# Kernel optimization log

Hardware: AMD Instinct MI355X
Metric: run time of the kernel (lower is better)

The kernel has to match this reference:

```python
import jax, jax.numpy as jnp
import numpy as np

N = 102400      # total agents across all groups
GROUP = 50      # agents per group
G = N // GROUP  # 2048 groups
E = 128         # embedding_dim
H = 512         # h_dim


def setup_inputs() -> dict:
    key = jax.random.key(0)
    k1, k2, k3, k4, k5, k6 = jax.random.split(key, 6)
    hist_enc = jax.random.normal(k1, (N, H), dtype=jnp.float32)
    hist_pos_batch = jax.random.normal(k2, (N, 2), dtype=jnp.float32)
    # group boundaries: 0, 50, 100, ..., N  (len = G+1)
    seq_start_end = (jnp.arange(G + 1, dtype=jnp.int32) * GROUP)
    # spatial_embedding: Linear(2, E)
    Ws = jax.random.normal(k3, (2, E), dtype=jnp.float32) * (1.0 / np.sqrt(2.0))
    bs = jax.random.normal(k4, (E,), dtype=jnp.float32) * 0.01
    # mlp_pre_pool: Linear(E + H, H)
    Wm = jax.random.normal(k5, (E + H, H), dtype=jnp.float32) * (1.0 / np.sqrt(E + H))
    bm = jax.random.normal(k6, (H,), dtype=jnp.float32) * 0.01
    return {
        "hist_enc": hist_enc,
        "hist_pos_batch": hist_pos_batch,
        "seq_start_end": seq_start_end,
        "Ws": Ws, "bs": bs, "Wm": Wm, "bm": bm,
    }


def reference(hist_enc, hist_pos_batch, seq_start_end, Ws, bs, Wm, bm):
    # The original torch loop builds all n^2 pairs per group but keeps only
    # curr_pool_h[0:1], i.e. row i=0 -> pooled vector for the group's FIRST agent.
    # rel[i=0, j] = pos[j] - pos[start]; hidden index is j; max over j.
    n = hist_enc.shape[0]
    num_groups = seq_start_end.shape[0] - 1
    # segment id of each agent: group g covers [sse[g], sse[g+1])
    seg_ids = jnp.searchsorted(seq_start_end, jnp.arange(n, dtype=seq_start_end.dtype), side="right") - 1
    starts = seq_start_end[:-1]                      # [G]
    anchor = hist_pos_batch[starts][seg_ids]         # [N,2] pos of group's first agent
    rel = hist_pos_batch - anchor                    # [N,2]
    emb = jax.nn.relu(rel @ Ws + bs)                 # [N,E]
    h_in = jnp.concatenate([hist_enc, emb], axis=1)  # [N,E+H]
    pooled = jax.nn.relu(h_in @ Wm + bm)             # [N,H]
    out = jax.ops.segment_max(pooled, seg_ids, num_segments=num_groups)  # [G,H]
    return out
```

## Files before the change

kernel.cpp:

```cpp
#include <hip/hip_runtime.h>


typedef __bf16 bf16x8 __attribute__((ext_vector_type(8)));
typedef float floatx4 __attribute__((ext_vector_type(4)));

constexpr int NR = 102400;
constexpr int NG = 2048;
constexpr int E  = 128;
constexpr int H  = 512;
constexpr int KD = 640;
constexpr int BM = 128, BN = 128, BK = 32;

__device__ inline unsigned short f2bf(float f) {
    unsigned u = __float_as_uint(f);
    u += 0x7FFF + ((u >> 16) & 1u);
    return (unsigned short)(u >> 16);
}

__device__ inline void async16(const void* g, void* l) {
    __builtin_amdgcn_global_load_lds(
        (const __attribute__((address_space(1))) unsigned int*)g,
        (__attribute__((address_space(3))) unsigned int*)l, 16, 0, 0);
}

__global__ __launch_bounds__(256) void wm_transpose(const float* __restrict__ Wm,
                                                    unsigned short* __restrict__ WmT) {
    __shared__ float tile[64][65];
    const int kb = blockIdx.x * 64, nb = blockIdx.y * 64;
    const int tx = threadIdx.x & 63, tq = threadIdx.x >> 6;
#pragma unroll
    for (int i = 0; i < 16; ++i) {
        const int k = tq * 16 + i;
        tile[k][tx] = Wm[(size_t)(kb + k) * H + nb + tx];
    }
    __syncthreads();
#pragma unroll
    for (int i = 0; i < 16; ++i) {
        const int n = tq * 16 + i;
        WmT[(size_t)(nb + n) * KD + kb + tx] = f2bf(tile[tx][n]);
    }
}

__global__ __launch_bounds__(256) void build_a(
    const float* __restrict__ hist_enc, const float* __restrict__ pos,
    const int* __restrict__ sse, const float* __restrict__ Ws,
    const float* __restrict__ bs, unsigned short* __restrict__ Abf)
{
    __shared__ float relRow[BM][2];
    const int t = threadIdx.x;
    const int rowBase = blockIdx.x * BM;
    if (t < BM) {
        const int i = rowBase + t;
        int l = 0, r = NG + 1;
        while (l < r) { int m = (l + r) >> 1; if (sse[m] <= i) l = m + 1; else r = m; }
        const int a = sse[l - 1];
        relRow[t][0] = pos[2 * i + 0] - pos[2 * a + 0];
        relRow[t][1] = pos[2 * i + 1] - pos[2 * a + 1];
    }
    __syncthreads();
#pragma unroll 4
    for (int j = 0; j < 32; ++j) {
        const int c = j * 256 + t;
        const int row = c >> 6, col = (c & 63) * 8;
        const float4 f0 = *(const float4*)&hist_enc[(size_t)(rowBase + row) * H + col];
        const float4 f1 = *(const float4*)&hist_enc[(size_t)(rowBase + row) * H + col + 4];
        unsigned short ub[8] = {f2bf(f0.x), f2bf(f0.y), f2bf(f0.z), f2bf(f0.w),
                                f2bf(f1.x), f2bf(f1.y), f2bf(f1.z), f2bf(f1.w)};
        *(uint4*)&Abf[(size_t)(rowBase + row) * KD + col] = *(const uint4*)ub;
    }
#pragma unroll 2
    for (int j = 0; j < 8; ++j) {
        const int c = j * 256 + t;
        const int row = c >> 4, e = (c & 15) * 8;
        const float r0 = relRow[row][0], r1 = relRow[row][1];
        const float4 w0a = *(const float4*)&Ws[e],     w0b = *(const float4*)&Ws[e + 4];
        const float4 w1a = *(const float4*)&Ws[E + e], w1b = *(const float4*)&Ws[E + e + 4];
        const float4 ba  = *(const float4*)&bs[e],     bb  = *(const float4*)&bs[e + 4];
        unsigned short ub[8] = {
            f2bf(fmaxf(r0 * w0a.x + r1 * w1a.x + ba.x, 0.f)),
            f2bf(fmaxf(r0 * w0a.y + r1 * w1a.y + ba.y, 0.f)),
            f2bf(fmaxf(r0 * w0a.z + r1 * w1a.z + ba.z, 0.f)),
            f2bf(fmaxf(r0 * w0a.w + r1 * w1a.w + ba.w, 0.f)),
            f2bf(fmaxf(r0 * w0b.x + r1 * w1b.x + bb.x, 0.f)),
            f2bf(fmaxf(r0 * w0b.y + r1 * w1b.y + bb.y, 0.f)),
            f2bf(fmaxf(r0 * w0b.z + r1 * w1b.z + bb.z, 0.f)),
            f2bf(fmaxf(r0 * w0b.w + r1 * w1b.w + bb.w, 0.f))};
        *(uint4*)&Abf[(size_t)(rowBase + row) * KD + H + e] = *(const uint4*)ub;
    }
}

__global__ __launch_bounds__(256) void pool_mfma4(
    const unsigned short* __restrict__ Abf,
    const int*   __restrict__ sse,
    const unsigned short* __restrict__ WmT,
    const float* __restrict__ bm,
    float*       __restrict__ out)
{
    __shared__ __attribute__((aligned(16))) unsigned short As2[2][BM * BK];
    __shared__ __attribute__((aligned(16))) unsigned short Bs2[2][BN * BK];
    __shared__ int segRow[BM];
    __shared__ int bnd[3];
    __shared__ int Pmax[4][BN + 4];

    const int t = threadIdx.x;
    const int bid     = blockIdx.x;
    const int rowTile = (bid >> 5) * 8 + (bid & 7);
    const int colTile = (bid >> 3) & 3;
    const int rowBase = rowTile * BM;
    const int cTile   = colTile * BN;

    const int lane  = t & 63;
    const int wv    = t >> 6;
    const int wr    = (wv >> 1) * 64;
    const int wc    = (wv & 1) * 64;
    const int lcol  = lane & 15;
    const int lquad = lane >> 4;

    const int sRow0 = wv * 32 + (lane >> 2);
    const int sRow1 = sRow0 + 16;
    const int phys  = lane & 3;
    const int cl0   = phys ^ ((sRow0 >> 1) & 3);
    const int cl1   = phys ^ ((sRow1 >> 1) & 3);
    const unsigned short* gA0 = Abf + (size_t)(rowBase + sRow0) * KD + cl0 * 8;
    const unsigned short* gA1 = Abf + (size_t)(rowBase + sRow1) * KD + cl1 * 8;
    const unsigned short* gB0 = WmT + (size_t)(cTile + sRow0) * KD + cl0 * 8;
    const unsigned short* gB1 = WmT + (size_t)(cTile + sRow1) * KD + cl1 * 8;

    auto issue = [&](int kt, int buf) {
        const int ko = kt * BK;
        async16(gA0 + ko, &As2[buf][wv * 1024]);
        async16(gA1 + ko, &As2[buf][wv * 1024 + 512]);
        async16(gB0 + ko, &Bs2[buf][wv * 1024]);
        async16(gB1 + ko, &Bs2[buf][wv * 1024 + 512]);
    };

    issue(0, 0);

    if (t < BM) {
        const int i = rowBase + t;
        int l = 0, r = NG + 1;
        while (l < r) { int m = (l + r) >> 1; if (sse[m] <= i) l = m + 1; else r = m; }
        segRow[t] = l - 1;
    }
    if (t >= BM && t < BM + 3) bnd[t - BM] = BM;
    for (int idx = t; idx < 4 * (BN + 4); idx += 256) ((int*)Pmax)[idx] = 0;
    __syncthreads();
    if (t < BM - 1) {
        const int s0 = segRow[t], s1 = segRow[t + 1];
        if (s1 != s0) bnd[s1 - segRow[0] - 1] = t + 1;
    }

    floatx4 acc[4][4];
#pragma unroll
    for (int m = 0; m < 4; ++m)
#pragma unroll
        for (int n = 0; n < 4; ++n) acc[m][n] = (floatx4){0.f, 0.f, 0.f, 0.f};

    for (int kt = 0; kt < KD / BK; ++kt) {
        __syncthreads();
        if (kt < KD / BK - 1) issue(kt + 1, (kt + 1) & 1);

        const unsigned short* A = As2[kt & 1];
        const unsigned short* B = Bs2[kt & 1];
        bf16x8 af[4], bfr[4];
#pragma unroll
        for (int mt = 0; mt < 4; ++mt) {
            const int R = wr + mt * 16 + lcol;
            const int pc = lquad ^ ((R >> 1) & 3);
            af[mt] = *(const bf16x8*)&A[R * 32 + pc * 8];
        }
#pragma unroll
        for (int nt = 0; nt < 4; ++nt) {
            const int R = wc + nt * 16 + lcol;
            const int pc = lquad ^ ((R >> 1) & 3);
            bfr[nt] = *(const bf16x8*)&B[R * 32 + pc * 8];
        }
#pragma unroll
        for (int mt = 0; mt < 4; ++mt)
#pragma unroll
            for (int nt = 0; nt < 4; ++nt)
                acc[mt][nt] = __builtin_amdgcn_mfma_f32_16x16x32_bf16(af[mt], bfr[nt], acc[mt][nt], 0, 0, 0);
    }

    const int b0 = bnd[0], b1 = bnd[1], b2 = bnd[2];
    const int segBase = segRow[0];

#pragma unroll
    for (int nt = 0; nt < 4; ++nt) {
        const int col  = wc + nt * 16 + lcol;
        const float bias = bm[cTile + col];
        float pm[4] = {0.f, 0.f, 0.f, 0.f};
#pragma unroll
        for (int mt = 0; mt < 4; ++mt) {
#pragma unroll
            for (int r = 0; r < 4; ++r) {
                const int lr = wr + mt * 16 + lquad * 4 + r;
                const int ls = (lr >= b0) + (lr >= b1) + (lr >= b2);
                const float v = fmaxf(acc[mt][nt][r] + bias, 0.f);
                pm[ls] = fmaxf(pm[ls], v);
            }
        }
#pragma unroll
        for (int ls = 0; ls < 4; ++ls)
            if (pm[ls] > 0.f)
                atomicMax(&Pmax[ls][col], __float_as_int(pm[ls]));
    }
    __syncthreads();

    for (int idx = t; idx < 4 * BN; idx += 256) {
        const int ls = idx >> 7, col = idx & 127;
        if (ls > 0 && bnd[ls - 1] >= BM) continue;
        const int seg = segBase + ls;
        const int v   = Pmax[ls][col];
        const int gs  = sse[seg], ge = sse[seg + 1];
        float* dst = &out[(size_t)seg * H + cTile + col];
        if (gs >= rowBase && ge <= rowBase + BM) {
            *dst = __int_as_float(v);
        } else {
            atomicMax((int*)dst, v);
        }
    }
}

constexpr int LDAF = 40;
__global__ __launch_bounds__(256) void pool_mfma_fb(
    const float* __restrict__ hist_enc, const float* __restrict__ pos,
    const int* __restrict__ sse, const float* __restrict__ Ws,
    const float* __restrict__ bs, const unsigned short* __restrict__ WmT,
    const float* __restrict__ bm, float* __restrict__ out)
{
    __shared__ __attribute__((aligned(16))) unsigned short As[BM][LDAF];
    __shared__ __attribute__((aligned(16))) unsigned short Bs[BN][LDAF];
    __shared__ float relRow[BM][2];
    __shared__ int   segRow[BM];
    __shared__ int   bnd[3];
    __shared__ int   Pmax[4][BN + 4];

    const int t = threadIdx.x;
    const int cTile = blockIdx.x * BN;
    const int rowBase = blockIdx.y * BM;

    if (t < BM) {
        const int i = rowBase + t;
        int l = 0, r = NG + 1;
        while (l < r) { int m = (l + r) >> 1; if (sse[m] <= i) l = m + 1; else r = m; }
        const int g = l - 1;
        segRow[t] = g;
        const int a = sse[g];
        relRow[t][0] = pos[2 * i + 0] - pos[2 * a + 0];
        relRow[t][1] = pos[2 * i + 1] - pos[2 * a + 1];
    }
    if (t >= BM && t < BM + 3) bnd[t - BM] = BM;
    for (int idx = t; idx < 4 * (BN + 4); idx += 256) ((int*)Pmax)[idx] = 0;
    __syncthreads();
    if (t < BM - 1) {
        const int s0 = segRow[t], s1 = segRow[t + 1];
        if (s1 != s0) bnd[s1 - segRow[0] - 1] = t + 1;
    }

    const int lane = t & 63, wv = t >> 6;
    const int wr = (wv >> 1) * 64, wc = (wv & 1) * 64;
    const int lcol = lane & 15, lquad = lane >> 4;

    floatx4 acc[4][4];
#pragma unroll
    for (int m = 0; m < 4; ++m)
#pragma unroll
        for (int n = 0; n < 4; ++n) acc[m][n] = (floatx4){0.f, 0.f, 0.f, 0.f};

    for (int kt = 0; kt < KD / BK; ++kt) {
        const int k0 = kt * BK;
        float4 av[4]; uint4 bv[2];
        if (k0 < H) {
#pragma unroll
            for (int i = 0; i < 4; ++i) {
                const int idx = i * 256 + t;
                const int row = idx >> 3, kq = (idx & 7) * 4;
                av[i] = *(const float4*)&hist_enc[(size_t)(rowBase + row) * H + k0 + kq];
            }
        } else {
#pragma unroll
            for (int i = 0; i < 4; ++i) {
                const int idx = i * 256 + t;
                const int row = idx >> 3, kq = (idx & 7) * 4;
                const int e = k0 - H + kq;
                const float4 w0 = *(const float4*)&Ws[e];
                const float4 w1 = *(const float4*)&Ws[E + e];
                const float4 b4 = *(const float4*)&bs[e];
                const float r0 = relRow[row][0], r1 = relRow[row][1];
                av[i].x = fmaxf(r0 * w0.x + r1 * w1.x + b4.x, 0.f);
                av[i].y = fmaxf(r0 * w0.y + r1 * w1.y + b4.y, 0.f);
                av[i].z = fmaxf(r0 * w0.z + r1 * w1.z + b4.z, 0.f);
                av[i].w = fmaxf(r0 * w0.w + r1 * w1.w + b4.w, 0.f);
            }
        }
#pragma unroll
        for (int i = 0; i < 2; ++i) {
            const int idx = i * 256 + t;
            const int n = idx >> 2, q = idx & 3;
            bv[i] = *(const uint4*)&WmT[(size_t)(cTile + n) * KD + k0 + q * 8];
        }
        __syncthreads();
#pragma unroll
        for (int i = 0; i < 4; ++i) {
            const int idx = i * 256 + t;
            const int row = idx >> 3, kq = (idx & 7) * 4;
            ushort4 p;
            p.x = f2bf(av[i].x); p.y = f2bf(av[i].y);
            p.z = f2bf(av[i].z); p.w = f2bf(av[i].w);
            *(ushort4*)&As[row][kq] = p;
        }
#pragma unroll
        for (int i = 0; i < 2; ++i) {
            const int idx = i * 256 + t;
            const int n = idx >> 2, q = idx & 3;
            *(uint4*)&Bs[n][q * 8] = bv[i];
        }
        __syncthreads();

        bf16x8 af[4], bfr[4];
#pragma unroll
        for (int mt = 0; mt < 4; ++mt)
            af[mt] = *(const bf16x8*)&As[wr + mt * 16 + lcol][lquad * 8];
#pragma unroll
        for (int nt = 0; nt < 4; ++nt)
            bfr[nt] = *(const bf16x8*)&Bs[wc + nt * 16 + lcol][lquad * 8];
#pragma unroll
        for (int mt = 0; mt < 4; ++mt)
#pragma unroll
            for (int nt = 0; nt < 4; ++nt)
                acc[mt][nt] = __builtin_amdgcn_mfma_f32_16x16x32_bf16(af[mt], bfr[nt], acc[mt][nt], 0, 0, 0);
    }

    const int b0 = bnd[0], b1 = bnd[1], b2 = bnd[2];
    const int segBase = segRow[0];
#pragma unroll
    for (int nt = 0; nt < 4; ++nt) {
        const int col = wc + nt * 16 + lcol;
        const float bias = bm[cTile + col];
        float pm[4] = {0.f, 0.f, 0.f, 0.f};
#pragma unroll
        for (int mt = 0; mt < 4; ++mt) {
#pragma unroll
            for (int r = 0; r < 4; ++r) {
                const int lr = wr + mt * 16 + lquad * 4 + r;
                const int ls = (lr >= b0) + (lr >= b1) + (lr >= b2);
                const float v = fmaxf(acc[mt][nt][r] + bias, 0.f);
                pm[ls] = fmaxf(pm[ls], v);
            }
        }
#pragma unroll
        for (int ls = 0; ls < 4; ++ls)
            if (pm[ls] > 0.f) atomicMax(&Pmax[ls][col], __float_as_int(pm[ls]));
    }
    __syncthreads();
    for (int idx = t; idx < 4 * BN; idx += 256) {
        const int ls = idx >> 7, col = idx & 127;
        if (ls > 0 && bnd[ls - 1] >= BM) continue;
        const int seg = segBase + ls;
        const int v = Pmax[ls][col];
        const int gs = sse[seg], ge = sse[seg + 1];
        float* dst = &out[(size_t)seg * H + cTile + col];
        if (gs >= rowBase && ge <= rowBase + BM) *dst = __int_as_float(v);
        else atomicMax((int*)dst, v);
    }
}

extern "C" void kernel_launch(void* const* d_in, const int* in_sizes, int n_in,
                              void* d_out, int out_size, void* d_ws, size_t ws_size,
                              hipStream_t stream) {
    const float* hist_enc = (const float*)d_in[0];
    const float* pos      = (const float*)d_in[1];
    const int*   sse      = (const int*)  d_in[2];
    const float* Ws       = (const float*)d_in[3];
    const float* bs       = (const float*)d_in[4];
    const float* Wm       = (const float*)d_in[5];
    const float* bm       = (const float*)d_in[6];
    float*       out      = (float*)d_out;

    const size_t needWmT = (size_t)H * KD * 2;
    const size_t needA   = (size_t)NR * KD * 2;
    unsigned short* WmT  = (unsigned short*)d_ws;

    hipMemsetAsync(out, 0, (size_t)out_size * sizeof(float), stream);
    wm_transpose<<<dim3(KD / 64, H / 64), 256, 0, stream>>>(Wm, WmT);

    if (ws_size >= needWmT + needA) {
        unsigned short* Abf = (unsigned short*)((char*)d_ws + needWmT);
        build_a<<<NR / BM, 256, 0, stream>>>(hist_enc, pos, sse, Ws, bs, Abf);
        pool_mfma4<<<3200, 256, 0, stream>>>(Abf, sse, WmT, bm, out);
    } else {
        pool_mfma_fb<<<dim3(H / BN, NR / BM), 256, 0, stream>>>(hist_enc, pos, sse, Ws, bs, WmT, bm, out);
    }
}
```

Baseline: 488.6 us.

## Triple-buffer GEMM K-loop with vmcnt waits and merge prep kernels

The weight transpose and the A-matrix build kernels become one prep launch, with block ranges picking the role, which saves a kernel launch. The pooled GEMM kernel moves from double to triple LDS buffering, issuing loads two K-tiles ahead. The per-iteration __syncthreads before the loads is replaced by an inline s_waitcnt vmcnt(4)/s_barrier after the MFMAs, so the next tile's loads can stay in flight. This uses more LDS, which may lower occupancy, and relies on hand-written wait counts being correct.

```diff
diff --git a/kernel.cpp b/kernel.cpp
--- a/kernel.cpp
+++ b/kernel.cpp
@@ -10,6 +10,7 @@
 constexpr int H  = 512;
 constexpr int KD = 640;
 constexpr int BM = 128, BN = 128, BK = 32;
+constexpr int KT = KD / BK;
 
 __device__ inline unsigned short f2bf(float f) {
     unsigned u = __float_as_uint(f);
@@ -23,81 +24,84 @@
         (__attribute__((address_space(3))) unsigned int*)l, 16, 0, 0);
 }
 
-__global__ __launch_bounds__(256) void wm_transpose(const float* __restrict__ Wm,
-                                                    unsigned short* __restrict__ WmT) {
-    __shared__ float tile[64][65];
-    const int kb = blockIdx.x * 64, nb = blockIdx.y * 64;
-    const int tx = threadIdx.x & 63, tq = threadIdx.x >> 6;
-#pragma unroll
-    for (int i = 0; i < 16; ++i) {
-        const int k = tq * 16 + i;
-        tile[k][tx] = Wm[(size_t)(kb + k) * H + nb + tx];
-    }
-    __syncthreads();
-#pragma unroll
-    for (int i = 0; i < 16; ++i) {
-        const int n = tq * 16 + i;
-        WmT[(size_t)(nb + n) * KD + kb + tx] = f2bf(tile[tx][n]);
-    }
-}
-
-__global__ __launch_bounds__(256) void build_a(
+__global__ __launch_bounds__(256) void prep(
     const float* __restrict__ hist_enc, const float* __restrict__ pos,
     const int* __restrict__ sse, const float* __restrict__ Ws,
-    const float* __restrict__ bs, unsigned short* __restrict__ Abf)
+    const float* __restrict__ bs, const float* __restrict__ Wm,
+    unsigned short* __restrict__ WmT, unsigned short* __restrict__ Abf, int doAbf)
 {
-    __shared__ float relRow[BM][2];
+    const int b = blockIdx.x;
     const int t = threadIdx.x;
-    const int rowBase = blockIdx.x * BM;
-    if (t < BM) {
-        const int i = rowBase + t;
-        int l = 0, r = NG + 1;
-        while (l < r) { int m = (l + r) >> 1; if (sse[m] <= i) l = m + 1; else r = m; }
-        const int a = sse[l - 1];
-        relRow[t][0] = pos[2 * i + 0] - pos[2 * a + 0];
-        relRow[t][1] = pos[2 * i + 1] - pos[2 * a + 1];
-    }
-    __syncthreads();
+    if (doAbf && b < 800) {
+        __shared__ float relRow[BM][2];
+        const int rowBase = b * BM;
+        if (t < BM) {
+            const int i = rowBase + t;
+            int l = 0, r = NG + 1;
+            while (l < r) { int m = (l + r) >> 1; if (sse[m] <= i) l = m + 1; else r = m; }
+            const int a = sse[l - 1];
+            relRow[t][0] = pos[2 * i + 0] - pos[2 * a + 0];
+            relRow[t][1] = pos[2 * i + 1] - pos[2 * a + 1];
+        }
+        __syncthreads();
 #pragma unroll 4
-    for (int j = 0; j < 32; ++j) {
-        const int c = j * 256 + t;
-        const int row = c >> 6, col = (c & 63) * 8;
-        const float4 f0 = *(const float4*)&hist_enc[(size_t)(rowBase + row) * H + col];
-        const float4 f1 = *(const float4*)&hist_enc[(size_t)(rowBase + row) * H + col + 4];
-        unsigned short ub[8] = {f2bf(f0.x), f2bf(f0.y), f2bf(f0.z), f2bf(f0.w),
-                                f2bf(f1.x), f2bf(f1.y), f2bf(f1.z), f2bf(f1.w)};
-        *(uint4*)&Abf[(size_t)(rowBase + row) * KD + col] = *(const uint4*)ub;
-    }
+        for (int j = 0; j < 32; ++j) {
+            const int c = j * 256 + t;
+            const int row = c >> 6, col = (c & 63) * 8;
+            const float4 f0 = *(const float4*)&hist_enc[(size_t)(rowBase + row) * H + col];
+            const float4 f1 = *(const float4*)&hist_enc[(size_t)(rowBase + row) * H + col + 4];
+            unsigned short ub[8] = {f2bf(f0.x), f2bf(f0.y), f2bf(f0.z), f2bf(f0.w),
+                                    f2bf(f1.x), f2bf(f1.y), f2bf(f1.z), f2bf(f1.w)};
+            *(uint4*)&Abf[(size_t)(rowBase + row) * KD + col] = *(const uint4*)ub;
+        }
 #pragma unroll 2
-    for (int j = 0; j < 8; ++j) {
-        const int c = j * 256 + t;
-        const int row = c >> 4, e = (c & 15) * 8;
-        const float r0 = relRow[row][0], r1 = relRow[row][1];
-        const float4 w0a = *(const float4*)&Ws[e],     w0b = *(const float4*)&Ws[e + 4];
-        const float4 w1a = *(const float4*)&Ws[E + e], w1b = *(const float4*)&Ws[E + e + 4];
-        const float4 ba  = *(const float4*)&bs[e],     bb  = *(const float4*)&bs[e + 4];
-        unsigned short ub[8] = {
-            f2bf(fmaxf(r0 * w0a.x + r1 * w1a.x + ba.x, 0.f)),
-            f2bf(fmaxf(r0 * w0a.y + r1 * w1a.y + ba.y, 0.f)),
-            f2bf(fmaxf(r0 * w0a.z + r1 * w1a.z + ba.z, 0.f)),
-            f2bf(fmaxf(r0 * w0a.w + r1 * w1a.w + ba.w, 0.f)),
-            f2bf(fmaxf(r0 * w0b.x + r1 * w1b.x + bb.x, 0.f)),
-            f2bf(fmaxf(r0 * w0b.y + r1 * w1b.y + bb.y, 0.f)),
-            f2bf(fmaxf(r0 * w0b.z + r1 * w1b.z + bb.z, 0.f)),
-            f2bf(fmaxf(r0 * w0b.w + r1 * w1b.w + bb.w, 0.f))};
-        *(uint4*)&Abf[(size_t)(rowBase + row) * KD + H + e] = *(const uint4*)ub;
-    }
-}
-
-__global__ __launch_bounds__(256) void pool_mfma4(
+        for (int j = 0; j < 8; ++j) {
+            const int c = j * 256 + t;
+            const int row = c >> 4, e = (c & 15) * 8;
+            const float r0 = relRow[row][0], r1 = relRow[row][1];
+            const float4 w0a = *(const float4*)&Ws[e],     w0b = *(const float4*)&Ws[e + 4];
+            const float4 w1a = *(const float4*)&Ws[E + e], w1b = *(const float4*)&Ws[E + e + 4];
+            const float4 ba  = *(const float4*)&bs[e],     bb  = *(const float4*)&bs[e + 4];
+            unsigned short ub[8] = {
+                f2bf(fmaxf(r0 * w0a.x + r1 * w1a.x + ba.x, 0.f)),
+                f2bf(fmaxf(r0 * w0a.y + r1 * w1a.y + ba.y, 0.f)),
+                f2bf(fmaxf(r0 * w0a.z + r1 * w1a.z + ba.z, 0.f)),
+                f2bf(fmaxf(r0 * w0a.w + r1 * w1a.w + ba.w, 0.f)),
+                f2bf(fmaxf(r0 * w0b.x + r1 * w1b.x + bb.x, 0.f)),
+                f2bf(fmaxf(r0 * w0b.y + r1 * w1b.y + bb.y, 0.f)),
+                f2bf(fmaxf(r0 * w0b.z + r1 * w1b.z + bb.z, 0.f)),
+                f2bf(fmaxf(r0 * w0b.w + r1 * w1b.w + bb.w, 0.f))};
+            *(uint4*)&Abf[(size_t)(rowBase + row) * KD + H + e] = *(const uint4*)ub;
+        }
+    } else {
+        const int bb = doAbf ? (b - 800) : b;
+        if (bb < 0 || bb >= 80) return;
+        __shared__ float tile[64][65];
+        const int kb = (bb % 10) * 64, nb = (bb / 10) * 64;
+        const int tx = t & 63, tq = t >> 6;
+#pragma unroll
+        for (int i = 0; i < 16; ++i) {
+            const int k = tq * 16 + i;
+            tile[k][tx] = Wm[(size_t)(kb + k) * H + nb + tx];
+        }
+        __syncthreads();
+#pragma unroll
+        for (int i = 0; i < 16; ++i) {
+            const int n = tq * 16 + i;
+            WmT[(size_t)(nb + n) * KD + kb + tx] = f2bf(tile[tx][n]);
+        }
+    }
+}
+
+__global__ __launch_bounds__(256) void pool_mfma5(
     const unsigned short* __restrict__ Abf,
     const int*   __restrict__ sse,
     const unsigned short* __restrict__ WmT,
     const float* __restrict__ bm,
     float*       __restrict__ out)
 {
-    __shared__ __attribute__((aligned(16))) unsigned short As2[2][BM * BK];
-    __shared__ __attribute__((aligned(16))) unsigned short Bs2[2][BN * BK];
+    __shared__ __attribute__((aligned(16))) unsigned short As3[3][BM * BK];
+    __shared__ __attribute__((aligned(16))) unsigned short Bs3[3][BN * BK];
     __shared__ int segRow[BM];
     __shared__ int bnd[3];
     __shared__ int Pmax[4][BN + 4];
@@ -126,15 +130,17 @@
     const unsigned short* gB0 = WmT + (size_t)(cTile + sRow0) * KD + cl0 * 8;
     const unsigned short* gB1 = WmT + (size_t)(cTile + sRow1) * KD + cl1 * 8;
 
-    auto issue = [&](int kt, int buf) {
-        const int ko = kt * BK;
-        async16(gA0 + ko, &As2[buf][wv * 1024]);
-        async16(gA1 + ko, &As2[buf][wv * 1024 + 512]);
-        async16(gB0 + ko, &Bs2[buf][wv * 1024]);
-        async16(gB1 + ko, &Bs2[buf][wv * 1024 + 512]);
+    auto issue = [&](int kt) {
+        const int buf = kt % 3;
+        const int ko  = kt * BK;
+        async16(gA0 + ko, &As3[buf][wv * 1024]);
+        async16(gA1 + ko, &As3[buf][wv * 1024 + 512]);
+        async16(gB0 + ko, &Bs3[buf][wv * 1024]);
+        async16(gB1 + ko, &Bs3[buf][wv * 1024 + 512]);
     };
 
-    issue(0, 0);
+    issue(0);
+    issue(1);
 
     if (t < BM) {
         const int i = rowBase + t;
@@ -156,12 +162,11 @@
 #pragma unroll
         for (int n = 0; n < 4; ++n) acc[m][n] = (floatx4){0.f, 0.f, 0.f, 0.f};
 
-    for (int kt = 0; kt < KD / BK; ++kt) {
-        __syncthreads();
-        if (kt < KD / BK - 1) issue(kt + 1, (kt + 1) & 1);
-
-        const unsigned short* A = As2[kt & 1];
-        const unsigned short* B = Bs2[kt & 1];
+    for (int kt = 0; kt < KT; ++kt) {
+        if (kt + 2 < KT) issue(kt + 2);
+
+        const unsigned short* A = As3[kt % 3];
+        const unsigned short* B = Bs3[kt % 3];
         bf16x8 af[4], bfr[4];
 #pragma unroll
         for (int mt = 0; mt < 4; ++mt) {
@@ -180,6 +185,12 @@
 #pragma unroll
             for (int nt = 0; nt < 4; ++nt)
                 acc[mt][nt] = __builtin_amdgcn_mfma_f32_16x16x32_bf16(af[mt], bfr[nt], acc[mt][nt], 0, 0, 0);
+
+        if (kt + 2 < KT) {
+            asm volatile("s_waitcnt vmcnt(4) lgkmcnt(0)\n\ts_barrier" ::: "memory");
+        } else {
+            asm volatile("s_waitcnt vmcnt(0) lgkmcnt(0)\n\ts_barrier" ::: "memory");
+        }
     }
 
     const int b0 = bnd[0], b1 = bnd[1], b2 = bnd[2];
@@ -381,15 +392,15 @@
     const size_t needWmT = (size_t)H * KD * 2;
     const size_t needA   = (size_t)NR * KD * 2;
     unsigned short* WmT  = (unsigned short*)d_ws;
+    unsigned short* Abf  = (unsigned short*)((char*)d_ws + needWmT);
 
     hipMemsetAsync(out, 0, (size_t)out_size * sizeof(float), stream);
-    wm_transpose<<<dim3(KD / 64, H / 64), 256, 0, stream>>>(Wm, WmT);
 
     if (ws_size >= needWmT + needA) {
-        unsigned short* Abf = (unsigned short*)((char*)d_ws + needWmT);
-        build_a<<<NR / BM, 256, 0, stream>>>(hist_enc, pos, sse, Ws, bs, Abf);
-        pool_mfma4<<<3200, 256, 0, stream>>>(Abf, sse, WmT, bm, out);
+        prep<<<880, 256, 0, stream>>>(hist_enc, pos, sse, Ws, bs, Wm, WmT, Abf, 1);
+        pool_mfma5<<<3200, 256, 0, stream>>>(Abf, sse, WmT, bm, out);
     } else {
+        prep<<<80, 256, 0, stream>>>(hist_enc, pos, sse, Ws, bs, Wm, WmT, Abf, 0);
         pool_mfma_fb<<<dim3(H / BN, NR / BM), 256, 0, stream>>>(hist_enc, pos, sse, Ws, bs, WmT, bm, out);
     }
 }
```

New measurement: 504.9 us. 3.3% more time.
